# Performance work log

Measured on AMD Instinct MI355X. Metric: run time of the kernel, lower is better.

The kernel has to match this reference:

```python
import jax, jax.numpy as jnp
import numpy as np

BN_EPS = 1e-5
SAMPLE_KEY = jax.random.key(42)


def setup_inputs() -> dict:
    key = jax.random.key(0)
    ks = jax.random.split(key, 12)
    B, W, E = 524288, 8, 4
    D = W * E  # 32, input dim of fc1

    def lin(k, fan_in, fan_out):
        k1, k2 = jax.random.split(k)
        bound = 1.0 / np.sqrt(fan_in)
        w = jax.random.uniform(k1, (fan_in, fan_out), jnp.float32, -bound, bound)
        b = jax.random.uniform(k2, (fan_out,), jnp.float32, -bound, bound)
        return w, b

    W1, b1 = lin(ks[0], D, 50)
    W2, b2 = lin(ks[1], 50, 30)
    W3, b3 = lin(ks[2], 30, 20)
    W4, b4 = lin(ks[3], 20, 15)
    W5, b5 = lin(ks[4], 15, W)
    # BatchNorm affine params (eval mode, running_mean=0, running_var=1)
    g1, be1 = jnp.ones((50,), jnp.float32), jnp.zeros((50,), jnp.float32)
    g2, be2 = jnp.ones((30,), jnp.float32), jnp.zeros((30,), jnp.float32)
    g3, be3 = jnp.ones((20,), jnp.float32), jnp.zeros((20,), jnp.float32)
    events = jax.random.normal(ks[5], (B, W, E), jnp.float32)
    return {"events": events,
            "W1": W1, "b1": b1, "g1": g1, "be1": be1,
            "W2": W2, "b2": b2, "g2": g2, "be2": be2,
            "W3": W3, "b3": b3, "g3": g3, "be3": be3,
            "W4": W4, "b4": b4, "W5": W5, "b5": b5}


def _bn_eval(x, g, b):
    # eval-mode BatchNorm1d with running_mean=0, running_var=1
    return x * (g / jnp.sqrt(1.0 + BN_EPS)) + b


def _probs(events, W1, b1, g1, be1, W2, b2, g2, be2, W3, b3, g3, be3, W4, b4, W5, b5):
    B = events.shape[0]
    x = events.reshape(B, -1)  # (B, window*event_size)
    h = jax.nn.relu(_bn_eval(x @ W1 + b1, g1, be1))
    h = jax.nn.relu(_bn_eval(h @ W2 + b2, g2, be2))
    h = jax.nn.relu(_bn_eval(h @ W3 + b3, g3, be3))
    h = jax.nn.relu(h @ W4 + b4)
    return jax.nn.sigmoid(h @ W5 + b5)  # (B, window_size)


def reference(events, W1, b1, g1, be1, W2, b2, g2, be2, W3, b3, g3, be3, W4, b4, W5, b5):
    p = _probs(events, W1, b1, g1, be1, W2, b2, g2, be2, W3, b3, g3, be3, W4, b4, W5, b5)
    # np.random.choice([0,1], p=[p, 1-p]) => P(choice=1) = 1 - p
    choice = jax.random.bernoulli(SAMPLE_KEY, 1.0 - p).astype(p.dtype)  # (B, W)
    chosen_events_np = 1.0 - choice
    flipped = jnp.abs(choice - p)            # prob of sampled outcome per element
    log_prob = jnp.log(jnp.prod(flipped, axis=1))  # (B,)
    return chosen_events_np, log_prob
```

## Files before the change

kernel.cpp:

```cpp
#include <hip/hip_runtime.h>
#include <math.h>

#define THREADS 256
#define TPW 4
#define ROWS_PER_BLOCK 256
#define P_MARGIN 2e-4f
#define FIXCAP 64

typedef float f32x4 __attribute__((ext_vector_type(4)));
typedef short short8 __attribute__((ext_vector_type(8)));
union Frag { unsigned u[4]; short8 s; };

#define FR1 0
#define FR2 2048
#define FR3 4096
#define FR4 5120
#define FR5 6144
#define VB1 6656
#define VS1 6708
#define VE1 6760
#define VB2 6812
#define VS2 6844
#define VE2 6876
#define VB3 6908
#define VS3 6928
#define VE3 6948
#define VB4 6968
#define VB5 6984
#define PZ  6992
#define WPOOL 7024

__device__ __forceinline__ void tf2x32(unsigned x0, unsigned x1,
                                       unsigned &o0, unsigned &o1) {
  const unsigned k0 = 0u;
  const unsigned k1 = 42u;
  const unsigned k2 = 0x1BD11BDAu ^ k0 ^ k1;
  x0 += k0; x1 += k1;
#define TF_R(r) { x0 += x1; x1 = (x1 << (r)) | (x1 >> (32 - (r))); x1 ^= x0; }
  TF_R(13) TF_R(15) TF_R(26) TF_R(6)
  x0 += k1; x1 += k2 + 1u;
  TF_R(17) TF_R(29) TF_R(16) TF_R(24)
  x0 += k2; x1 += k0 + 2u;
  TF_R(13) TF_R(15) TF_R(26) TF_R(6)
  x0 += k0; x1 += k1 + 3u;
  TF_R(17) TF_R(29) TF_R(16) TF_R(24)
  x0 += k1; x1 += k2 + 4u;
  TF_R(13) TF_R(15) TF_R(26) TF_R(6)
  x0 += k2; x1 += k0 + 5u;
#undef TF_R
  o0 = x0; o1 = x1;
}

__device__ __forceinline__ unsigned rtnb(float v) {
  unsigned b = __float_as_uint(v);
  return (b + 0x7FFFu + ((b >> 16) & 1u)) & 0xFFFF0000u;
}

__device__ __forceinline__ unsigned cvtpk(float a, float b) {
  unsigned r;
  asm("v_cvt_pk_bf16_f32 %0, %1, %2" : "=v"(r) : "v"(a), "v"(b));
  return r;
}

__device__ __forceinline__ void pack8(const float f[8], short8 &H, short8 &L) {
  Frag h, l;
#pragma unroll
  for (int d = 0; d < 4; ++d) {
    unsigned hd = cvtpk(f[2 * d], f[2 * d + 1]);
    h.u[d] = hd;
    float r0 = f[2 * d]     - __uint_as_float(hd << 16);
    float r1 = f[2 * d + 1] - __uint_as_float(hd & 0xFFFF0000u);
    l.u[d] = cvtpk(r0, r1);
  }
  H = h.s; L = l.s;
}

__device__ __forceinline__ f32x4 mfma16(short8 a, short8 b, f32x4 c) {
  return __builtin_amdgcn_mfma_f32_16x16x32_bf16(a, b, c, 0, 0, 0);
}

__device__ __forceinline__ short8 ldfrag(const float *sW, int dwoff) {
  return *reinterpret_cast<const short8 *>(sW + dwoff);
}
__device__ __forceinline__ f32x4 ldv4(const float *sW, int dwoff) {
  return *reinterpret_cast<const f32x4 *>(sW + dwoff);
}

template <int K, int N, int NT, int FB, bool PERM>
__device__ __forceinline__ void stageA(const float *__restrict__ W,
                                       float *sW, int t) {
  for (int i = t; i < K * N; i += THREADS) {
    int k = i / N, n = i - k * N;
    float v = W[i];
    unsigned hb = rtnb(v);
    unsigned lb = rtnb(v - __uint_as_float(hb));
    int kt = k >> 5, g = (k >> 3) & 3, e = k & 7, d = e >> 1, par = e & 1;
    int tile, r;
    if (PERM) {
      int pg = n >> 5, m = n & 31, tt = (m >> 2) & 1;
      r = ((m >> 3) << 2) | (m & 3);
      tile = pg * 2 + tt;
    } else {
      tile = n >> 4; r = n & 15;
    }
    int lane = g * 16 + r;
    int dwhi = FB + (kt * NT + tile) * 512 + lane * 4 + d;
    unsigned short *hp = reinterpret_cast<unsigned short *>(sW);
    hp[2 * dwhi + par] = (unsigned short)(hb >> 16);
    hp[2 * (dwhi + 256) + par] = (unsigned short)(lb >> 16);
  }
}

__device__ __forceinline__ void bnpack(f32x4 a0, f32x4 a1, const float *sW,
                                       int vs, int ve, int g,
                                       short8 &H, short8 &L) {
  f32x4 sc0 = ldv4(sW, vs + g * 8),     of0 = ldv4(sW, ve + g * 8);
  f32x4 sc1 = ldv4(sW, vs + g * 8 + 4), of1 = ldv4(sW, ve + g * 8 + 4);
  float f[8];
#pragma unroll
  for (int q = 0; q < 4; ++q) {
    f[q]     = fmaxf(fmaf(a0[q], sc0[q], of0[q]), 0.f);
    f[4 + q] = fmaxf(fmaf(a1[q], sc1[q], of1[q]), 0.f);
  }
  pack8(f, H, L);
}

__global__ __launch_bounds__(THREADS, 2)
void wtf_kernel(const float* __restrict__ events,
                const float* __restrict__ W1, const float* __restrict__ b1,
                const float* __restrict__ g1, const float* __restrict__ be1,
                const float* __restrict__ W2, const float* __restrict__ b2,
                const float* __restrict__ g2, const float* __restrict__ be2,
                const float* __restrict__ W3, const float* __restrict__ b3,
                const float* __restrict__ g3, const float* __restrict__ be3,
                const float* __restrict__ W4, const float* __restrict__ b4,
                const float* __restrict__ W5, const float* __restrict__ b5,
                float* __restrict__ out_chosen,
                float* __restrict__ out_logp,
                int B) {
  __shared__ float sW[WPOOL];
  __shared__ unsigned s_cnt;
  __shared__ unsigned s_rows[FIXCAP];
  __shared__ double sA[64];
  __shared__ double sB[64];
  __shared__ double sF[8];

  const int t = threadIdx.x;
  const float rden = (float)(1.0 / sqrt(1.0 + 1e-5));

  if (t == 0) s_cnt = 0;
  for (int i = t; i < WPOOL; i += THREADS) sW[i] = 0.f;
  __syncthreads();
  stageA<32, 50, 4, FR1, true>(W1, sW, t);
  stageA<50, 30, 2, FR2, true>(W2, sW, t);
  stageA<30, 20, 2, FR3, true>(W3, sW, t);
  stageA<20, 15, 2, FR4, true>(W4, sW, t);
  stageA<15,  8, 1, FR5, false>(W5, sW, t);
  if (t < 50)                  { sW[VB1 + t] = b1[t]; sW[VS1 + t] = g1[t] * rden; sW[VE1 + t] = be1[t]; }
  else if (t >= 64 && t < 94)  { int i = t - 64;  sW[VB2 + i] = b2[i]; sW[VS2 + i] = g2[i] * rden; sW[VE2 + i] = be2[i]; }
  else if (t >= 128 && t < 148){ int i = t - 128; sW[VB3 + i] = b3[i]; sW[VS3 + i] = g3[i] * rden; sW[VE3 + i] = be3[i]; }
  else if (t >= 192 && t < 207){ sW[VB4 + (t - 192)] = b4[t - 192]; }
  else if (t >= 224 && t < 232){ sW[VB5 + (t - 224)] = b5[t - 224]; }
  __syncthreads();

  const int w = t >> 6, lane = t & 63;
  const int c = lane & 15, g = lane >> 4;
  const int labase = lane * 4;

  const int wrow0 = blockIdx.x * ROWS_PER_BLOCK + w * (TPW * 16);
  const float4 *xp = reinterpret_cast<const float4 *>(
      events + (size_t)(wrow0 + c) * 32 + g * 8);
  float4 xa = xp[0], xb = xp[1];

#pragma unroll 1
  for (int tt = 0; tt < TPW; ++tt) {
    const int r0 = wrow0 + tt * 16;
    const int row = r0 + c;

    float xf[8] = {xa.x, xa.y, xa.z, xa.w, xb.x, xb.y, xb.z, xb.w};
    short8 Xh, Xl; pack8(xf, Xh, Xl);
    const int ttn = (tt + 1 < TPW) ? tt + 1 : tt;
    xa = xp[ttn * 128]; xb = xp[ttn * 128 + 1];

    f32x4 a1[4];
#pragma unroll
    for (int ti = 0; ti < 4; ++ti) {
      f32x4 acc = ldv4(sW, VB1 + (ti >> 1) * 32 + g * 8 + (ti & 1) * 4);
      short8 wh = ldfrag(sW, FR1 + ti * 512 + labase);
      short8 wl = ldfrag(sW, FR1 + ti * 512 + 256 + labase);
      acc = mfma16(wh, Xl, acc);
      acc = mfma16(wl, Xh, acc);
      a1[ti] = mfma16(wh, Xh, acc);
    }

    short8 B2h[2], B2l[2];
    bnpack(a1[0], a1[1], sW, VS1,      VE1,      g, B2h[0], B2l[0]);
    bnpack(a1[2], a1[3], sW, VS1 + 32, VE1 + 32, g, B2h[1], B2l[1]);

    f32x4 a2[2];
#pragma unroll
    for (int ti = 0; ti < 2; ++ti) {
      f32x4 acc = ldv4(sW, VB2 + g * 8 + ti * 4);
#pragma unroll
      for (int kt = 0; kt < 2; ++kt) {
        short8 wh = ldfrag(sW, FR2 + (kt * 2 + ti) * 512 + labase);
        short8 wl = ldfrag(sW, FR2 + (kt * 2 + ti) * 512 + 256 + labase);
        acc = mfma16(wh, B2l[kt], acc);
        acc = mfma16(wl, B2h[kt], acc);
        acc = mfma16(wh, B2h[kt], acc);
      }
      a2[ti] = acc;
    }

    short8 B3h, B3l;
    bnpack(a2[0], a2[1], sW, VS2, VE2, g, B3h, B3l);

    f32x4 a3[2];
#pragma unroll
    for (int ti = 0; ti < 2; ++ti) {
      f32x4 acc = ldv4(sW, VB3 + g * 8 + ti * 4);
      short8 wh = ldfrag(sW, FR3 + ti * 512 + labase);
      short8 wl = ldfrag(sW, FR3 + ti * 512 + 256 + labase);
      acc = mfma16(wh, B3l, acc);
      acc = mfma16(wl, B3h, acc);
      a3[ti] = mfma16(wh, B3h, acc);
    }

    short8 B4h, B4l;
    bnpack(a3[0], a3[1], sW, VS3, VE3, g, B4h, B4l);

    f32x4 a4[2];
#pragma unroll
    for (int ti = 0; ti < 2; ++ti) {
      f32x4 acc = ldv4(sW, VB4 + g * 8 + ti * 4);
      short8 wh = ldfrag(sW, FR4 + ti * 512 + labase);
      short8 wl = ldfrag(sW, FR4 + ti * 512 + 256 + labase);
      acc = mfma16(wh, B4l, acc);
      acc = mfma16(wl, B4h, acc);
      a4[ti] = mfma16(wh, B4h, acc);
    }

    short8 B5h, B5l;
    {
      float f[8];
#pragma unroll
      for (int q = 0; q < 4; ++q) {
        f[q]     = fmaxf(a4[0][q], 0.f);
        f[4 + q] = fmaxf(a4[1][q], 0.f);
      }
      pack8(f, B5h, B5l);
    }

    f32x4 a5;
    {
      f32x4 acc = ldv4(sW, VB5 + g * 4);
      short8 wh = ldfrag(sW, FR5 + labase);
      short8 wl = ldfrag(sW, FR5 + 256 + labase);
      acc = mfma16(wh, B5l, acc);
      acc = mfma16(wl, B5h, acc);
      a5 = mfma16(wh, B5h, acc);
    }

    {
      float s2v = __shfl_xor(a5[2], 32);
      float s3v = __shfl_xor(a5[3], 32);
      float l0 = (g < 2) ? a5[0] : s2v;
      float l1 = (g < 2) ? a5[1] : s3v;
      const int base = ((g & 1) << 2) | ((g >> 1) << 1);
      float p0 = 1.f / (1.f + __expf(-l0));
      float p1 = 1.f / (1.f + __expf(-l1));
      unsigned o0, o1, q0, q1;
      tf2x32(0u, 8u * (unsigned)row + (unsigned)base,      o0, o1);
      tf2x32(0u, 8u * (unsigned)row + (unsigned)base + 1u, q0, q1);
      float u0 = __uint_as_float(0x3F800000u | ((o0 ^ o1) >> 9)) - 1.f;
      float u1 = __uint_as_float(0x3F800000u | ((q0 ^ q1) >> 9)) - 1.f;
      float th0 = 1.f - p0, th1 = 1.f - p1;
      bool c0 = u0 < th0, c1 = u1 < th1;
      bool need = (fabsf(u0 - th0) < P_MARGIN) || (fabsf(u1 - th1) < P_MARGIN);
      float prod = (c0 ? th0 : p0) * (c1 ? th1 : p1);
      prod *= __shfl_xor(prod, 16);
      prod *= __shfl_xor(prod, 32);
      float2 chv = make_float2(c0 ? 0.f : 1.f, c1 ? 0.f : 1.f);
      *reinterpret_cast<float2 *>(out_chosen + (size_t)row * 8 + base) = chv;
      if (g == 0) out_logp[row] = __logf(prod);
      if (need) {
        unsigned i = atomicAdd(&s_cnt, 1u);
        if (i < FIXCAP) s_rows[i] = (unsigned)row;
      }
    }
  }

  __syncthreads();
  unsigned cnt = s_cnt;
  if (cnt > FIXCAP) cnt = FIXCAP;
  if (cnt == 0) return;

  const double denom = sqrt(1.0 + 1e-5);
  for (unsigned r = 0; r < cnt; ++r) {
    const int rb = (int)s_rows[r];

    if (t < 32) sA[t] = (double)events[(size_t)rb * 32 + t];
    __syncthreads();

    double v = 0.0;
    if (t < 50) {
#pragma unroll
      for (int k = 0; k < 32; ++k) v = fma(sA[k], (double)W1[k * 50 + t], v);
      v += (double)b1[t];
      v = v * ((double)g1[t] / denom) + (double)be1[t];
      v = v > 0.0 ? v : 0.0;
    }
    __syncthreads();
    if (t < 50) sB[t] = v;
    __syncthreads();

    v = 0.0;
    if (t < 30) {
#pragma unroll
      for (int k = 0; k < 50; ++k) v = fma(sB[k], (double)W2[k * 30 + t], v);
      v += (double)b2[t];
      v = v * ((double)g2[t] / denom) + (double)be2[t];
      v = v > 0.0 ? v : 0.0;
    }
    __syncthreads();
    if (t < 30) sA[t] = v;
    __syncthreads();

    v = 0.0;
    if (t < 20) {
#pragma unroll
      for (int k = 0; k < 30; ++k) v = fma(sA[k], (double)W3[k * 20 + t], v);
      v += (double)b3[t];
      v = v * ((double)g3[t] / denom) + (double)be3[t];
      v = v > 0.0 ? v : 0.0;
    }
    __syncthreads();
    if (t < 20) sB[t] = v;
    __syncthreads();

    v = 0.0;
    if (t < 15) {
#pragma unroll
      for (int k = 0; k < 20; ++k) v = fma(sB[k], (double)W4[k * 15 + t], v);
      v += (double)b4[t];
      v = v > 0.0 ? v : 0.0;
    }
    __syncthreads();
    if (t < 15) sA[t] = v;
    __syncthreads();

    if (t < 8) {
      v = 0.0;
#pragma unroll
      for (int k = 0; k < 15; ++k) v = fma(sA[k], (double)W5[k * 8 + t], v);
      v += (double)b5[t];
      double p = 1.0 / (1.0 + exp(-v));
      unsigned j = 8u * (unsigned)rb + (unsigned)t, o0, o1;
      tf2x32(0u, j, o0, o1);
      unsigned bits = o0 ^ o1;
      float u = __uint_as_float(0x3F800000u | (bits >> 9)) - 1.f;
      double thr = 1.0 - p;
      bool choice = ((double)u < thr);
      out_chosen[(size_t)rb * 8 + t] = choice ? 0.f : 1.f;
      sF[t] = choice ? thr : p;
    }
    __syncthreads();
    if (t == 0) {
      double prod = 1.0;
      for (int w2 = 0; w2 < 8; ++w2) prod *= sF[w2];
      out_logp[rb] = (float)log(prod);
    }
    __syncthreads();
  }
}

extern "C" void kernel_launch(void* const* d_in, const int* in_sizes, int n_in,
                              void* d_out, int out_size, void* d_ws, size_t ws_size,
                              hipStream_t stream) {
  const float* events = (const float*)d_in[0];
  const float* W1  = (const float*)d_in[1];
  const float* b1  = (const float*)d_in[2];
  const float* g1  = (const float*)d_in[3];
  const float* be1 = (const float*)d_in[4];
  const float* W2  = (const float*)d_in[5];
  const float* b2  = (const float*)d_in[6];
  const float* g2  = (const float*)d_in[7];
  const float* be2 = (const float*)d_in[8];
  const float* W3  = (const float*)d_in[9];
  const float* b3  = (const float*)d_in[10];
  const float* g3  = (const float*)d_in[11];
  const float* be3 = (const float*)d_in[12];
  const float* W4  = (const float*)d_in[13];
  const float* b4  = (const float*)d_in[14];
  const float* W5  = (const float*)d_in[15];
  const float* b5  = (const float*)d_in[16];

  const int B = in_sizes[0] / 32;
  float* out = (float*)d_out;
  float* out_chosen = out;
  float* out_logp   = out + (size_t)B * 8;

  const int blocks = (B + ROWS_PER_BLOCK - 1) / ROWS_PER_BLOCK;
  hipLaunchKernelGGL(wtf_kernel, dim3(blocks), dim3(THREADS), 0, stream,
                     events, W1, b1, g1, be1, W2, b2, g2, be2,
                     W3, b3, g3, be3, W4, b4, W5, b5,
                     out_chosen, out_logp, B);
}
```

Before: 222.9 us.

## Process two 16-row tiles per iteration to interleave MFMA chains and reuse weight fragments

```diff
diff --git a/kernel.cpp b/kernel.cpp
--- a/kernel.cpp
+++ b/kernel.cpp
@@ -2,8 +2,8 @@
 #include <math.h>
 
 #define THREADS 256
-#define TPW 4
-#define ROWS_PER_BLOCK 256
+#define TPW 8
+#define ROWS_PER_BLOCK 512
 #define P_MARGIN 2e-4f
 #define FIXCAP 64
 
@@ -170,102 +170,143 @@
   const int wrow0 = blockIdx.x * ROWS_PER_BLOCK + w * (TPW * 16);
   const float4 *xp = reinterpret_cast<const float4 *>(
       events + (size_t)(wrow0 + c) * 32 + g * 8);
-  float4 xa = xp[0], xb = xp[1];
+  float4 xA0 = xp[0], xA1 = xp[1], xB0 = xp[128], xB1 = xp[129];
 
 #pragma unroll 1
-  for (int tt = 0; tt < TPW; ++tt) {
-    const int r0 = wrow0 + tt * 16;
-    const int row = r0 + c;
-
-    float xf[8] = {xa.x, xa.y, xa.z, xa.w, xb.x, xb.y, xb.z, xb.w};
-    short8 Xh, Xl; pack8(xf, Xh, Xl);
-    const int ttn = (tt + 1 < TPW) ? tt + 1 : tt;
-    xa = xp[ttn * 128]; xb = xp[ttn * 128 + 1];
-
-    f32x4 a1[4];
+  for (int it = 0; it < TPW / 2; ++it) {
+    const int rA = wrow0 + it * 32;
+    const int rB = rA + 16;
+
+    short8 Xh[2], Xl[2];
+    {
+      float fA[8] = {xA0.x, xA0.y, xA0.z, xA0.w, xA1.x, xA1.y, xA1.z, xA1.w};
+      float fB[8] = {xB0.x, xB0.y, xB0.z, xB0.w, xB1.x, xB1.y, xB1.z, xB1.w};
+      pack8(fA, Xh[0], Xl[0]);
+      pack8(fB, Xh[1], Xl[1]);
+    }
+    {
+      const int nit = (it + 1 < TPW / 2) ? it + 1 : it;
+      const int nx = nit * 256;
+      xA0 = xp[nx]; xA1 = xp[nx + 1]; xB0 = xp[nx + 128]; xB1 = xp[nx + 129];
+    }
+
+    f32x4 a1[2][4];
 #pragma unroll
     for (int ti = 0; ti < 4; ++ti) {
-      f32x4 acc = ldv4(sW, VB1 + (ti >> 1) * 32 + g * 8 + (ti & 1) * 4);
       short8 wh = ldfrag(sW, FR1 + ti * 512 + labase);
       short8 wl = ldfrag(sW, FR1 + ti * 512 + 256 + labase);
-      acc = mfma16(wh, Xl, acc);
-      acc = mfma16(wl, Xh, acc);
-      a1[ti] = mfma16(wh, Xh, acc);
-    }
-
-    short8 B2h[2], B2l[2];
-    bnpack(a1[0], a1[1], sW, VS1,      VE1,      g, B2h[0], B2l[0]);
-    bnpack(a1[2], a1[3], sW, VS1 + 32, VE1 + 32, g, B2h[1], B2l[1]);
-
-    f32x4 a2[2];
+      f32x4 bias = ldv4(sW, VB1 + (ti >> 1) * 32 + g * 8 + (ti & 1) * 4);
+#pragma unroll
+      for (int u = 0; u < 2; ++u) {
+        f32x4 acc = bias;
+        acc = mfma16(wh, Xl[u], acc);
+        acc = mfma16(wl, Xh[u], acc);
+        a1[u][ti] = mfma16(wh, Xh[u], acc);
+      }
+    }
+
+    short8 B2h[2][2], B2l[2][2];
+#pragma unroll
+    for (int u = 0; u < 2; ++u) {
+      bnpack(a1[u][0], a1[u][1], sW, VS1,      VE1,      g, B2h[u][0], B2l[u][0]);
+      bnpack(a1[u][2], a1[u][3], sW, VS1 + 32, VE1 + 32, g, B2h[u][1], B2l[u][1]);
+    }
+
+    f32x4 a2[2][2];
+#pragma unroll
+    for (int u = 0; u < 2; ++u) {
+      f32x4 b0 = ldv4(sW, VB2 + g * 8);
+      f32x4 b1v = ldv4(sW, VB2 + g * 8 + 4);
+      a2[u][0] = b0; a2[u][1] = b1v;
+    }
 #pragma unroll
     for (int ti = 0; ti < 2; ++ti) {
-      f32x4 acc = ldv4(sW, VB2 + g * 8 + ti * 4);
 #pragma unroll
       for (int kt = 0; kt < 2; ++kt) {
         short8 wh = ldfrag(sW, FR2 + (kt * 2 + ti) * 512 + labase);
         short8 wl = ldfrag(sW, FR2 + (kt * 2 + ti) * 512 + 256 + labase);
-        acc = mfma16(wh, B2l[kt], acc);
-        acc = mfma16(wl, B2h[kt], acc);
-        acc = mfma16(wh, B2h[kt], acc);
-      }
-      a2[ti] = acc;
-    }
-
-    short8 B3h, B3l;
-    bnpack(a2[0], a2[1], sW, VS2, VE2, g, B3h, B3l);
-
-    f32x4 a3[2];
+#pragma unroll
+        for (int u = 0; u < 2; ++u) {
+          a2[u][ti] = mfma16(wh, B2l[u][kt], a2[u][ti]);
+          a2[u][ti] = mfma16(wl, B2h[u][kt], a2[u][ti]);
+          a2[u][ti] = mfma16(wh, B2h[u][kt], a2[u][ti]);
+        }
+      }
+    }
+
+    short8 B3h[2], B3l[2];
+#pragma unroll
+    for (int u = 0; u < 2; ++u)
+      bnpack(a2[u][0], a2[u][1], sW, VS2, VE2, g, B3h[u], B3l[u]);
+
+    f32x4 a3[2][2];
 #pragma unroll
     for (int ti = 0; ti < 2; ++ti) {
-      f32x4 acc = ldv4(sW, VB3 + g * 8 + ti * 4);
       short8 wh = ldfrag(sW, FR3 + ti * 512 + labase);
       short8 wl = ldfrag(sW, FR3 + ti * 512 + 256 + labase);
-      acc = mfma16(wh, B3l, acc);
-      acc = mfma16(wl, B3h, acc);
-      a3[ti] = mfma16(wh, B3h, acc);
-    }
-
-    short8 B4h, B4l;
-    bnpack(a3[0], a3[1], sW, VS3, VE3, g, B4h, B4l);
-
-    f32x4 a4[2];
+      f32x4 bias = ldv4(sW, VB3 + g * 8 + ti * 4);
+#pragma unroll
+      for (int u = 0; u < 2; ++u) {
+        f32x4 acc = bias;
+        acc = mfma16(wh, B3l[u], acc);
+        acc = mfma16(wl, B3h[u], acc);
+        a3[u][ti] = mfma16(wh, B3h[u], acc);
+      }
+    }
+
+    short8 B4h[2], B4l[2];
+#pragma unroll
+    for (int u = 0; u < 2; ++u)
+      bnpack(a3[u][0], a3[u][1], sW, VS3, VE3, g, B4h[u], B4l[u]);
+
+    f32x4 a4[2][2];
 #pragma unroll
     for (int ti = 0; ti < 2; ++ti) {
-      f32x4 acc = ldv4(sW, VB4 + g * 8 + ti * 4);
       short8 wh = ldfrag(sW, FR4 + ti * 512 + labase);
       short8 wl = ldfrag(sW, FR4 + ti * 512 + 256 + labase);
-      acc = mfma16(wh, B4l, acc);
-      acc = mfma16(wl, B4h, acc);
-      a4[ti] = mfma16(wh, B4h, acc);
-    }
-
-    short8 B5h, B5l;
+      f32x4 bias = ldv4(sW, VB4 + g * 8 + ti * 4);
+#pragma unroll
+      for (int u = 0; u < 2; ++u) {
+        f32x4 acc = bias;
+        acc = mfma16(wh, B4l[u], acc);
+        acc = mfma16(wl, B4h[u], acc);
+        a4[u][ti] = mfma16(wh, B4h[u], acc);
+      }
+    }
+
+    short8 B5h[2], B5l[2];
+#pragma unroll
+    for (int u = 0; u < 2; ++u) {
+      float f[8];
+#pragma unroll
+      for (int q = 0; q < 4; ++q) {
+        f[q]     = fmaxf(a4[u][0][q], 0.f);
+        f[4 + q] = fmaxf(a4[u][1][q], 0.f);
+      }
+      pack8(f, B5h[u], B5l[u]);
+    }
+
+    f32x4 a5[2];
     {
-      float f[8];
-#pragma unroll
-      for (int q = 0; q < 4; ++q) {
-        f[q]     = fmaxf(a4[0][q], 0.f);
-        f[4 + q] = fmaxf(a4[1][q], 0.f);
-      }
-      pack8(f, B5h, B5l);
-    }
-
-    f32x4 a5;
-    {
-      f32x4 acc = ldv4(sW, VB5 + g * 4);
       short8 wh = ldfrag(sW, FR5 + labase);
       short8 wl = ldfrag(sW, FR5 + 256 + labase);
-      acc = mfma16(wh, B5l, acc);
-      acc = mfma16(wl, B5h, acc);
-      a5 = mfma16(wh, B5h, acc);
-    }
-
-    {
-      float s2v = __shfl_xor(a5[2], 32);
-      float s3v = __shfl_xor(a5[3], 32);
-      float l0 = (g < 2) ? a5[0] : s2v;
-      float l1 = (g < 2) ? a5[1] : s3v;
+      f32x4 bias = ldv4(sW, VB5 + g * 4);
+#pragma unroll
+      for (int u = 0; u < 2; ++u) {
+        f32x4 acc = bias;
+        acc = mfma16(wh, B5l[u], acc);
+        acc = mfma16(wl, B5h[u], acc);
+        a5[u] = mfma16(wh, B5h[u], acc);
+      }
+    }
+
+#pragma unroll
+    for (int u = 0; u < 2; ++u) {
+      const int row = (u ? rB : rA) + c;
+      float s2v = __shfl_xor(a5[u][2], 32);
+      float s3v = __shfl_xor(a5[u][3], 32);
+      float l0 = (g < 2) ? a5[u][0] : s2v;
+      float l1 = (g < 2) ? a5[u][1] : s3v;
       const int base = ((g & 1) << 2) | ((g >> 1) << 1);
       float p0 = 1.f / (1.f + __expf(-l0));
       float p1 = 1.f / (1.f + __expf(-l1));
```

After: 225.6 us. No clear change (+1.2%).
